# Performance work log

Measured on AMD Instinct MI355X. Metric: run time of the kernel, lower is better.

## Reference

```python
import jax, jax.numpy as jnp
import numpy as np

# ---- VoronoiDecoder constants (defaults from __init__) ----
EPS = 1e-8
W_MIN = 0.005
BETA = 0.02
RAW_TEMP = 5.0
H_MIN, H_MAX = 0.5, 2.0
J_BETA_SCALE = 1.0
J_WIDTH_BONUS = 0.15
J_KEFF_LAMBDA = 0.05
J_KEFF_K0 = 3.0
J_KEFF_S = 0.35
J_TRIPLE_LAMBDA = 0.15
J_TRIPLE_POWER = 1.5
GAP_THR_MIN, GAP_THR_MAX = 0.0, 0.5
BIG_THR_MIN, BIG_THR_MAX = 0.0, 0.6
ALPHA_MIN, ALPHA_MAX = 0.01, 0.2
ETA_MIN, ETA_MAX = 0.01, 0.2


def _map_raw(x, lo, hi):
    return lo + (hi - lo) * jax.nn.sigmoid(x)


def _forward(uv, seeds_raw, w_raw, h_raw, theta, a_raw,
             gap_thr_raw, big_thr_raw, alpha_raw, eta_raw):
    seeds = seeds_raw                                   # (S,2); seeds_uv is identity
    # pairwise seed distance (default buffers: single non-periodic face -> plain norm)
    v = seeds[:, None, :] - seeds[None, :, :]           # (S,S,2)
    pair_dist = jnp.sqrt(jnp.sum(v * v, axis=-1) + EPS)
    # width(): geometric clamp + sigmoid blend, symmetrized
    w_max_pair = jnp.maximum(0.8 * pair_dist, W_MIN + EPS)
    w_geo = W_MIN + (w_max_pair - W_MIN) * jax.nn.sigmoid(w_raw / RAW_TEMP)
    W = 0.5 * (w_geo + w_geo.T)                         # (S,S)
    # height(): bounded sigmoid
    h = H_MIN + (H_MAX - H_MIN) * jax.nn.sigmoid(h_raw[0])
    # anisotropic metric per seed: rotate by theta, scale by aspect a
    diff = uv[:, None, :] - seeds[None, :, :]           # (Q,S,2)
    c, s = jnp.cos(theta), jnp.sin(theta)               # (S,)
    du = c * diff[..., 0] + s * diff[..., 1]
    dv = -s * diff[..., 0] + c * diff[..., 1]
    a = 0.5 + 1.5 * jax.nn.sigmoid(a_raw)               # (S,) aspect ratio in (0.5,2)
    d = jnp.sqrt((du * a) ** 2 + (dv / a) ** 2 + EPS)   # (Q,S)
    # nearest / second-nearest seed (soft Voronoi wall field)
    neg2, idx2 = jax.lax.top_k(-d, 2)                   # (Q,2)
    d1 = -neg2[:, 0]
    d2 = -neg2[:, 1]
    gap = d2 - d1
    w_pair = W[idx2[:, 0], idx2[:, 1]]                  # (Q,)
    # junction gating via soft effective seed count keff
    p = jax.nn.softmax(-d / BETA, axis=-1)              # (Q,S)
    keff = 1.0 / (jnp.sum(p * p, axis=-1) + EPS)
    jfac = jax.nn.sigmoid((keff - J_KEFF_K0) / J_KEFF_S)
    w_eff = w_pair * (1.0 + J_WIDTH_BONUS * jfac)
    beta_eff = BETA * J_BETA_SCALE * (1.0 + J_KEFF_LAMBDA * jfac)
    wall = jax.nn.sigmoid((w_eff - gap) / beta_eff)
    # pair gating (use_pair_gating=True): suppress walls across large gaps
    gap_thr = _map_raw(gap_thr_raw[0], GAP_THR_MIN, GAP_THR_MAX)
    big_thr = _map_raw(big_thr_raw[0], BIG_THR_MIN, BIG_THR_MAX)
    alpha_g = _map_raw(alpha_raw[0], ALPHA_MIN, ALPHA_MAX)
    eta_g = _map_raw(eta_raw[0], ETA_MIN, ETA_MAX)
    gate = jax.nn.sigmoid((gap_thr - gap) / alpha_g) * jax.nn.sigmoid((big_thr - d1) / eta_g)
    # triple-junction bonus density
    triple = J_TRIPLE_LAMBDA * jnp.maximum(keff - J_KEFF_K0, 0.0) ** J_TRIPLE_POWER
    occ = jnp.clip(wall * gate + triple, 0.0, 1.0)
    return occ * h                                      # (Q,) thickness field


def setup_inputs() -> dict:
    key = jax.random.key(0)
    ks = jax.random.split(key, 10)
    Q, S = 65536, 512
    return {
        "uv": jax.random.uniform(ks[0], (Q, 2), dtype=jnp.float32),
        "seeds_raw": jax.random.uniform(ks[1], (S, 2), dtype=jnp.float32),
        "w_raw": jax.random.normal(ks[2], (S, S), dtype=jnp.float32),
        "h_raw": jax.random.normal(ks[3], (1,), dtype=jnp.float32),
        "theta": jax.random.normal(ks[4], (S,), dtype=jnp.float32),
        "a_raw": jax.random.normal(ks[5], (S,), dtype=jnp.float32),
        "gap_thr_raw": jax.random.normal(ks[6], (1,), dtype=jnp.float32),
        "big_thr_raw": jax.random.normal(ks[7], (1,), dtype=jnp.float32),
        "alpha_raw": jax.random.normal(ks[8], (1,), dtype=jnp.float32),
        "eta_raw": jax.random.normal(ks[9], (1,), dtype=jnp.float32),
    }


def reference(uv, seeds_raw, w_raw, h_raw, theta, a_raw,
              gap_thr_raw, big_thr_raw, alpha_raw, eta_raw):
    return _forward(uv, seeds_raw, w_raw, h_raw, theta, a_raw,
                    gap_thr_raw, big_thr_raw, alpha_raw, eta_raw)
```

## Files before the change

### kernel.cpp

```cpp
#include <hip/hip_runtime.h>
#include <math.h>

#define EPSF    1e-8f
#define W_MINF  0.005f
#define BETAF   0.02f
#define LOG2E   1.4426950408889634f

constexpr double KD    = 1.4426950408889634 / 0.02;
constexpr float  K2F   = (float)(KD * KD);
constexpr float  K2EPS = (float)(KD * KD * 1e-8);
constexpr float  INVK  = (float)(1.0 / KD);

__device__ __forceinline__ float fast_exp(float x) {
    return __builtin_amdgcn_exp2f(x * LOG2E);
}
__device__ __forceinline__ float sigm(float x) {
    return 1.0f / (1.0f + fast_exp(-x));
}
__device__ __forceinline__ float ex2(float x) { return __builtin_amdgcn_exp2f(x); }

extern "C" __global__ __launch_bounds__(512)
void seed_prep(const float* __restrict__ seeds,
               const float* __restrict__ theta,
               const float* __restrict__ a_raw,
               float* __restrict__ ws, int S)
{
    int j = blockIdx.x * blockDim.x + threadIdx.x;
    if (j >= S) return;
    float sx = seeds[2 * j + 0];
    float sy = seeds[2 * j + 1];
    float sn, cs;
    __sincosf(theta[j], &sn, &cs);
    float a   = 0.5f + 1.5f * sigm(a_raw[j]);
    float a2  = a * a;
    float ia2 = 1.0f / a2;
    float c2 = cs * cs, s2 = sn * sn;
    ws[0 * 512 + j] = sx;
    ws[1 * 512 + j] = sy;
    ws[2 * 512 + j] = K2F * (c2 * a2 + s2 * ia2);
    ws[3 * 512 + j] = K2F * (s2 * a2 + c2 * ia2);
    ws[4 * 512 + j] = K2F * (cs * sn * (a2 - ia2));
}

extern "C" __global__ __launch_bounds__(512)
void voronoi_kernel(const float* __restrict__ uv,
                    const float* __restrict__ w_raw,
                    const float* __restrict__ h_raw,
                    const float* __restrict__ gap_thr_raw,
                    const float* __restrict__ big_thr_raw,
                    const float* __restrict__ alpha_raw,
                    const float* __restrict__ eta_raw,
                    const float* __restrict__ ws,
                    float* __restrict__ out,
                    int Q, int S)
{
    const float* __restrict__ tx = ws + 0 * 512;
    const float* __restrict__ ty = ws + 1 * 512;
    const float* __restrict__ tA = ws + 2 * 512;
    const float* __restrict__ tB = ws + 3 * 512;
    const float* __restrict__ tC = ws + 4 * 512;

    const int part = __builtin_amdgcn_readfirstlane((int)(threadIdx.x >> 6));
    const int lane = threadIdx.x & 63;
    const int q    = blockIdx.x * 64 + lane;
    const int qc   = q < Q ? q : (Q - 1);

    const float ux = uv[2 * qc + 0];
    const float uy = uv[2 * qc + 1];

    unsigned v1 = 0x7F7FFFFFu, v2 = 0x7F7FFFFFu;
    float s1 = 0.0f, s2 = 0.0f;

    const int base = part * 64;
    #pragma unroll 8
    for (int t = 0; t < 64; ++t) {
        const int j = base + t;
        const float sx = tx[j], sy = ty[j];
        const float A = tA[j], B = tB[j], C = tC[j];
        float dx = ux - sx;
        float dy = uy - sy;
        float p  = fmaf(A, dx, C * dy);
        float qq = fmaf(C, dx, B * dy);
        float r  = fmaf(dx, p, fmaf(dy, qq, K2EPS));
        float d  = __builtin_amdgcn_sqrtf(r);

        unsigned pv  = (__float_as_uint(d) & 0xFFFFFE00u) | (unsigned)j;
        unsigned v1o = v1;
        v1 = v1 < pv ? v1 : pv;
        unsigned mx = v1o > pv ? v1o : pv;
        v2 = mx < v2 ? mx : v2;

        float mo = __uint_as_float(v1o);
        float mn = __uint_as_float(v1);
        float am = ex2(mn - mo);
        float bm = ex2(mn - d);
        s1 = fmaf(s1, am, bm);
        s2 = fmaf(s2, am * am, bm * bm);
    }

    __shared__ unsigned mv1[8][64], mv2[8][64];
    __shared__ float    ms1[8][64], ms2[8][64];
    mv1[part][lane] = v1;  mv2[part][lane] = v2;
    ms1[part][lane] = s1;  ms2[part][lane] = s2;
    __syncthreads();
    if (part != 0) return;

    unsigned V1 = mv1[0][lane], V2 = mv2[0][lane];
    float    S1 = ms1[0][lane], S2 = ms2[0][lane];
    #pragma unroll
    for (int p2 = 1; p2 < 8; ++p2) {
        unsigned w1 = mv1[p2][lane], w2 = mv2[p2][lane];
        float    t1 = ms1[p2][lane], t2 = ms2[p2][lane];
        unsigned n1 = V1 < w1 ? V1 : w1;
        unsigned hi = V1 > w1 ? V1 : w1;
        unsigned lo2 = V2 < w2 ? V2 : w2;
        unsigned n2 = hi < lo2 ? hi : lo2;
        float fa = ex2(__uint_as_float(n1) - __uint_as_float(V1));
        float fb = ex2(__uint_as_float(n1) - __uint_as_float(w1));
        S1 = fmaf(S1, fa, t1 * fb);
        S2 = fmaf(S2, fa * fa, t2 * (fb * fb));
        V1 = n1; V2 = n2;
    }

    const int i1 = (int)(V1 & 511u);
    const int i2 = (int)(V2 & 511u);
    float d1  = __uint_as_float(V1) * INVK;
    float gap = (__uint_as_float(V2) - __uint_as_float(V1)) * INVK;

    float sp2  = S2 / (S1 * S1);
    float keff = 1.0f / (sp2 + EPSF);
    float jfac = sigm((keff - 3.0f) * (1.0f / 0.35f));

    float ddx   = tx[i1] - tx[i2];
    float ddy   = ty[i1] - ty[i2];
    float pdist = __builtin_amdgcn_sqrtf(fmaf(ddx, ddx, fmaf(ddy, ddy, EPSF)));
    float wmax  = fmaxf(0.8f * pdist, W_MINF + EPSF);
    float sij   = sigm(w_raw[i1 * S + i2] * 0.2f);
    float sji   = sigm(w_raw[i2 * S + i1] * 0.2f);
    float wpair = W_MINF + (wmax - W_MINF) * 0.5f * (sij + sji);

    float weff     = wpair * fmaf(0.15f, jfac, 1.0f);
    float beta_eff = BETAF * fmaf(0.05f, jfac, 1.0f);
    float wall     = sigm((weff - gap) / beta_eff);

    float gap_thr = 0.5f  * sigm(gap_thr_raw[0]);
    float big_thr = 0.6f  * sigm(big_thr_raw[0]);
    float alpha_g = 0.01f + 0.19f * sigm(alpha_raw[0]);
    float eta_g   = 0.01f + 0.19f * sigm(eta_raw[0]);

    float gate = sigm((gap_thr - gap) / alpha_g) * sigm((big_thr - d1) / eta_g);

    float t      = fmaxf(keff - 3.0f, 0.0f);
    float triple = 0.15f * t * __builtin_amdgcn_sqrtf(t);

    float h   = 0.5f + 1.5f * sigm(h_raw[0]);
    float occ = fminf(fmaxf(fmaf(wall, gate, triple), 0.0f), 1.0f);
    if (q < Q) out[q] = occ * h;
}

extern "C" void kernel_launch(void* const* d_in, const int* in_sizes, int n_in,
                              void* d_out, int out_size, void* d_ws, size_t ws_size,
                              hipStream_t stream)
{
    const float* uv          = (const float*)d_in[0];
    const float* seeds_raw   = (const float*)d_in[1];
    const float* w_raw       = (const float*)d_in[2];
    const float* h_raw       = (const float*)d_in[3];
    const float* theta       = (const float*)d_in[4];
    const float* a_raw       = (const float*)d_in[5];
    const float* gap_thr_raw = (const float*)d_in[6];
    const float* big_thr_raw = (const float*)d_in[7];
    const float* alpha_raw   = (const float*)d_in[8];
    const float* eta_raw     = (const float*)d_in[9];
    float* out = (float*)d_out;
    float* ws  = (float*)d_ws;

    const int Q = in_sizes[0] / 2;
    const int S = in_sizes[4];

    seed_prep<<<dim3((S + 511) / 512), dim3(512), 0, stream>>>(seeds_raw, theta,
                                                               a_raw, ws, S);

    dim3 block(512);
    dim3 grid((Q + 63) / 64);
    voronoi_kernel<<<grid, block, 0, stream>>>(uv, w_raw, h_raw,
                                               gap_thr_raw, big_thr_raw,
                                               alpha_raw, eta_raw,
                                               ws, out, Q, S);
}
```

Measured before the change: 93.54 us.

## Drop online-softmax rescaling, rank by squared distance, pack FP32 math in pairs

```diff
diff --git a/kernel.cpp b/kernel.cpp
--- a/kernel.cpp
+++ b/kernel.cpp
@@ -10,6 +10,8 @@
 constexpr float  K2F   = (float)(KD * KD);
 constexpr float  K2EPS = (float)(KD * KD * 1e-8);
 constexpr float  INVK  = (float)(1.0 / KD);
+
+typedef float v2f __attribute__((ext_vector_type(2)));
 
 __device__ __forceinline__ float fast_exp(float x) {
     return __builtin_amdgcn_exp2f(x * LOG2E);
@@ -65,43 +67,57 @@
     const int q    = blockIdx.x * 64 + lane;
     const int qc   = q < Q ? q : (Q - 1);
 
-    const float ux = uv[2 * qc + 0];
-    const float uy = uv[2 * qc + 1];
-
-    unsigned v1 = 0x7F7FFFFFu, v2 = 0x7F7FFFFFu;
-    float s1 = 0.0f, s2 = 0.0f;
+    const float2 u = *reinterpret_cast<const float2*>(&uv[2 * qc]);
+    const v2f uxv = { u.x, u.x };
+    const v2f uyv = { u.y, u.y };
+    const v2f epsv = { K2EPS, K2EPS };
+
+    unsigned v1u = 0x7F7FFFFFu, v2u = 0x7F7FFFFFu;
+    v2f s1v = { 0.0f, 0.0f };
+    v2f s2v = { 0.0f, 0.0f };
 
     const int base = part * 64;
-    #pragma unroll 8
-    for (int t = 0; t < 64; ++t) {
+    #pragma unroll 4
+    for (int t = 0; t < 64; t += 2) {
         const int j = base + t;
-        const float sx = tx[j], sy = ty[j];
-        const float A = tA[j], B = tB[j], C = tC[j];
-        float dx = ux - sx;
-        float dy = uy - sy;
-        float p  = fmaf(A, dx, C * dy);
-        float qq = fmaf(C, dx, B * dy);
-        float r  = fmaf(dx, p, fmaf(dy, qq, K2EPS));
-        float d  = __builtin_amdgcn_sqrtf(r);
-
-        unsigned pv  = (__float_as_uint(d) & 0xFFFFFE00u) | (unsigned)j;
-        unsigned v1o = v1;
-        v1 = v1 < pv ? v1 : pv;
-        unsigned mx = v1o > pv ? v1o : pv;
-        v2 = mx < v2 ? mx : v2;
-
-        float mo = __uint_as_float(v1o);
-        float mn = __uint_as_float(v1);
-        float am = ex2(mn - mo);
-        float bm = ex2(mn - d);
-        s1 = fmaf(s1, am, bm);
-        s2 = fmaf(s2, am * am, bm * bm);
+        const v2f sx = *reinterpret_cast<const v2f*>(&tx[j]);
+        const v2f sy = *reinterpret_cast<const v2f*>(&ty[j]);
+        const v2f A  = *reinterpret_cast<const v2f*>(&tA[j]);
+        const v2f B  = *reinterpret_cast<const v2f*>(&tB[j]);
+        const v2f C  = *reinterpret_cast<const v2f*>(&tC[j]);
+
+        v2f dx = uxv - sx;
+        v2f dy = uyv - sy;
+        v2f p  = A * dx + C * dy;
+        v2f qq = C * dx + B * dy;
+        v2f r  = dx * p + (dy * qq + epsv);
+
+        float nd0 = -__builtin_amdgcn_sqrtf(r.x);
+        float nd1 = -__builtin_amdgcn_sqrtf(r.y);
+        v2f e = { ex2(nd0), ex2(nd1) };
+        s1v = s1v + e;
+        s2v = e * e + s2v;
+
+        unsigned pv0 = (__float_as_uint(r.x) & 0xFFFFFE00u) | (unsigned)j;
+        unsigned o0  = v1u;
+        v1u = v1u < pv0 ? v1u : pv0;
+        unsigned m0 = o0 > pv0 ? o0 : pv0;
+        v2u = m0 < v2u ? m0 : v2u;
+
+        unsigned pv1 = (__float_as_uint(r.y) & 0xFFFFFE00u) | (unsigned)(j + 1);
+        unsigned o1  = v1u;
+        v1u = v1u < pv1 ? v1u : pv1;
+        unsigned m1 = o1 > pv1 ? o1 : pv1;
+        v2u = m1 < v2u ? m1 : v2u;
     }
+
+    float s1 = s1v.x + s1v.y;
+    float s2 = s2v.x + s2v.y;
 
     __shared__ unsigned mv1[8][64], mv2[8][64];
     __shared__ float    ms1[8][64], ms2[8][64];
-    mv1[part][lane] = v1;  mv2[part][lane] = v2;
-    ms1[part][lane] = s1;  ms2[part][lane] = s2;
+    mv1[part][lane] = v1u;  mv2[part][lane] = v2u;
+    ms1[part][lane] = s1;   ms2[part][lane] = s2;
     __syncthreads();
     if (part != 0) return;
 
@@ -110,24 +126,23 @@
     #pragma unroll
     for (int p2 = 1; p2 < 8; ++p2) {
         unsigned w1 = mv1[p2][lane], w2 = mv2[p2][lane];
-        float    t1 = ms1[p2][lane], t2 = ms2[p2][lane];
+        S1 += ms1[p2][lane];
+        S2 += ms2[p2][lane];
         unsigned n1 = V1 < w1 ? V1 : w1;
         unsigned hi = V1 > w1 ? V1 : w1;
-        unsigned lo2 = V2 < w2 ? V2 : w2;
-        unsigned n2 = hi < lo2 ? hi : lo2;
-        float fa = ex2(__uint_as_float(n1) - __uint_as_float(V1));
-        float fb = ex2(__uint_as_float(n1) - __uint_as_float(w1));
-        S1 = fmaf(S1, fa, t1 * fb);
-        S2 = fmaf(S2, fa * fa, t2 * (fb * fb));
-        V1 = n1; V2 = n2;
+        unsigned l2 = V2 < w2 ? V2 : w2;
+        V2 = hi < l2 ? hi : l2;
+        V1 = n1;
     }
 
     const int i1 = (int)(V1 & 511u);
     const int i2 = (int)(V2 & 511u);
-    float d1  = __uint_as_float(V1) * INVK;
-    float gap = (__uint_as_float(V2) - __uint_as_float(V1)) * INVK;
-
-    float sp2  = S2 / (S1 * S1);
+    float d1K = __builtin_amdgcn_sqrtf(__uint_as_float(V1));
+    float d2K = __builtin_amdgcn_sqrtf(__uint_as_float(V2));
+    float d1  = d1K * INVK;
+    float gap = (d2K - d1K) * INVK;
+
+    float sp2  = (S2 / S1) / S1;
     float keff = 1.0f / (sp2 + EPSF);
     float jfac = sigm((keff - 3.0f) * (1.0f / 0.35f));
 
```

After: 87.21 us. 6.8% less time.
